# Performance work log

Hardware: AMD Instinct MI355X
Metric: run time of the kernel (lower is better)

## Reference

```python
import jax, jax.numpy as jnp
import numpy as np

B, N_PIC, C, H, W, P = 32, 4, 3, 224, 224, 16
HP = H // P  # 14
NP = HP * HP  # 196 patches
D = C * P * P  # 768 = hidden_size


def setup_inputs() -> dict:
    key = jax.random.key(0)
    ks = jax.random.split(key, 12)
    s = 0.02
    def lin(k, din, dout):
        kw, kb = jax.random.split(k)
        return (jax.random.normal(kw, (din, dout), jnp.float32) * s,
                jax.random.normal(kb, (dout,), jnp.float32) * s)
    W1, b1 = lin(ks[0], D, D)
    Wq, bq = lin(ks[1], D, D)
    Wk, bk = lin(ks[2], D, D)
    Wv, bv = lin(ks[3], D, D)
    Wo1, bo1 = lin(ks[4], D, D)
    Wo2, bo2 = lin(ks[5], D, D)
    x = jax.random.normal(ks[6], (B, N_PIC, C, H, W), jnp.float32)
    return {"x": x, "W1": W1, "b1": b1, "Wq": Wq, "bq": bq, "Wk": Wk,
            "bk": bk, "Wv": Wv, "bv": bv, "Wo1": Wo1, "bo1": bo1,
            "Wo2": Wo2, "bo2": bo2}


def reference(x, W1, b1, Wq, bq, Wk, bk, Wv, bv, Wo1, bo1, Wo2, bo2):
    b = x.shape[0]
    # patchify: matches torch unfold(3,P,P).unfold(4,P,P) + permute + view
    # -> [b, N, num_patches, C*P*P] with (C, ph, pw) ordering in last dim
    p = x.reshape(b, N_PIC, C, HP, P, HP, P)
    p = p.transpose(0, 1, 3, 5, 2, 4, 6).reshape(b, N_PIC, NP, D)
    h = p @ W1 + b1  # [b, N, S, D]
    # attention: query always from picture 0; key/value per picture (batched)
    Q = h[:, 0] @ Wq + bq          # [b, S, D]
    K = h @ Wk + bk                # [b, N, S, D]
    V = h @ Wv + bv                # [b, N, S, D]
    scale = 1.0 / jnp.sqrt(jnp.float32(D))
    scores = jnp.einsum('bsd,bnmd->bnsm', Q, K) * scale  # [b, N, S, S]
    attn = jax.nn.softmax(scores, axis=-1)
    wv = jnp.einsum('bnsm,bnmd->bnsd', attn, V)           # [b, N, S, D]
    out = jax.nn.relu(wv @ Wo1 + bo1) @ Wo2 + bo2
    return out
```

## Files before the change

kernel.cpp:

```cpp
#include <hip/hip_runtime.h>

typedef __bf16 bf16;
typedef __bf16 bf16x8 __attribute__((ext_vector_type(8)));
typedef float  f32x4  __attribute__((ext_vector_type(4)));


__global__ __launch_bounds__(256) void patchify_k(const float* __restrict__ x,
                                                  bf16* __restrict__ p) {
  int t = blockIdx.x * 256 + threadIdx.x;
  if (t >= 128 * 3 * 14 * 16 * 14) return;
  int j  = t % 14; t /= 14;
  int ph = t % 16; t /= 16;
  int i  = t % 14; t /= 14;
  int c  = t % 3;  t /= 3;
  int bn = t;
  const float* src = x + (((long long)(bn * 3 + c) * 224 + (i * 16 + ph)) * 224 + j * 16);
  bf16* dst = p + ((long long)(bn * 196 + (i * 14 + j)) * 768 + c * 256 + ph * 16);
  bf16 tmp[16];
  for (int k = 0; k < 16; k += 4) {
    float4 f = *(const float4*)(src + k);
    tmp[k + 0] = (bf16)f.x; tmp[k + 1] = (bf16)f.y;
    tmp[k + 2] = (bf16)f.z; tmp[k + 3] = (bf16)f.w;
  }
  *(bf16x8*)(dst)     = *(bf16x8*)&tmp[0];
  *(bf16x8*)(dst + 8) = *(bf16x8*)&tmp[8];
}

__global__ __launch_bounds__(256) void wtrans_k(const float* __restrict__ w0,
                                                const float* __restrict__ w1,
                                                const float* __restrict__ w2,
                                                const float* __restrict__ w3,
                                                const float* __restrict__ w4,
                                                const float* __restrict__ w5,
                                                bf16* __restrict__ out) {
  __shared__ float tile[32][33];
  const float* W;
  switch (blockIdx.z) {
    case 0: W = w0; break; case 1: W = w1; break; case 2: W = w2; break;
    case 3: W = w3; break; case 4: W = w4; break; default: W = w5; break;
  }
  bf16* o = out + (long long)blockIdx.z * 768 * 768;
  int nb = blockIdx.x * 32, kb = blockIdx.y * 32;
  int c = threadIdx.x & 31, r = threadIdx.x >> 5;
  for (int rr = 0; rr < 32; rr += 8)
    tile[r + rr][c] = W[(long long)(kb + r + rr) * 768 + nb + c];
  __syncthreads();
  for (int rr = 0; rr < 32; rr += 8)
    o[(long long)(nb + r + rr) * 768 + kb + c] = (bf16)tile[c][r + rr];
}

__global__ __launch_bounds__(256) void vtrans_k(const bf16* __restrict__ kv,
                                                bf16* __restrict__ Vt) {
  __shared__ short tile[32][33];
  int z = blockIdx.z;
  const short* v = (const short*)(kv + (long long)z * 301056 + 768);
  short* vt = (short*)(Vt + (long long)z * 768 * 224);
  int db = blockIdx.x * 32;
  int mb = blockIdx.y * 32;
  int c = threadIdx.x & 31, r = threadIdx.x >> 5;
  for (int rr = 0; rr < 32; rr += 8) {
    int m = mb + r + rr;
    short val = 0;
    if (m < 196) val = v[(long long)m * 1536 + db + c];
    tile[r + rr][c] = val;
  }
  __syncthreads();
  for (int rr = 0; rr < 32; rr += 8) {
    int d = db + r + rr;
    vt[(long long)d * 224 + mb + c] = tile[c][r + rr];
  }
}

__global__ __launch_bounds__(64) void softmax_k(const float* __restrict__ S,
                                                bf16* __restrict__ attn) {
  const int row = blockIdx.x;
  const float* sr = S + (long long)row * 196;
  const int l = threadIdx.x;
  float v0 = sr[l];
  float v1 = sr[l + 64];
  float v2 = sr[l + 128];
  float v3 = (l + 192 < 196) ? sr[l + 192] : -1e30f;
  float mx = fmaxf(fmaxf(v0, v1), fmaxf(v2, v3));
  for (int o = 32; o > 0; o >>= 1) mx = fmaxf(mx, __shfl_xor(mx, o));
  float e0 = __expf(v0 - mx);
  float e1 = __expf(v1 - mx);
  float e2 = __expf(v2 - mx);
  float e3 = (l + 192 < 196) ? __expf(v3 - mx) : 0.f;
  float s = e0 + e1 + e2 + e3;
  for (int o = 32; o > 0; o >>= 1) s += __shfl_xor(s, o);
  float inv = 1.0f / s;
  bf16* ar = attn + (long long)row * 224;
  ar[l]       = (bf16)(e0 * inv);
  ar[l + 64]  = (bf16)(e1 * inv);
  ar[l + 128] = (bf16)(e2 * inv);
  int m3 = l + 192;
  if (m3 < 196) ar[m3] = (bf16)(e3 * inv);
  else if (m3 < 224) ar[m3] = (bf16)0.0f;
}

__device__ __forceinline__ void gld16(const bf16* g, bf16* l) {
  __builtin_amdgcn_global_load_lds(
      (const __attribute__((address_space(1))) unsigned int*)g,
      (__attribute__((address_space(3))) unsigned int*)l, 16, 0, 0);
}

__global__ __launch_bounds__(256) void gemm128(
    const bf16* __restrict__ A, const bf16* __restrict__ Bt,
    const float* __restrict__ bias, const float* __restrict__ bias2,
    void* __restrict__ Cout,
    int M, int N, int K, int lda, int ldb, int gr, long long gs,
    long long strideAz, int a_zdiv, long long strideBz, long long strideCz,
    float scale, int relu, int out_bf16) {
  __shared__ __align__(16) char smem[34816];
  bf16* AsBuf = (bf16*)smem;
  bf16* BsBuf = (bf16*)(smem + 16384);

  const int tid = threadIdx.x;
  const int lane = tid & 63;
  const int w = tid >> 6;
  const int wm = w & 1, wn = w >> 1;
  const int z = blockIdx.z;
  const int n0 = blockIdx.x * 128, m0 = blockIdx.y * 128;

  const bf16* Az  = A  + (long long)(z / a_zdiv) * strideAz;
  const bf16* Btz = Bt + (long long)z * strideBz;

  const int rl  = 16 * w + (lane & 15);
  const int kc8 = (lane >> 4) * 8;
  int ar0 = m0 + rl;        if (ar0 >= M) ar0 = M - 1;
  int ar1 = m0 + 64 + rl;   if (ar1 >= M) ar1 = M - 1;
  const bf16* aP0 = Az + (long long)(ar0 / gr) * gs + (long long)(ar0 % gr) * lda + kc8;
  const bf16* aP1 = Az + (long long)(ar1 / gr) * gs + (long long)(ar1 % gr) * lda + kc8;
  int br0 = n0 + rl;        if (br0 >= N) br0 = N - 1;
  int br1 = n0 + 64 + rl;   if (br1 >= N) br1 = N - 1;
  const bf16* bP0 = Btz + (long long)br0 * ldb + kc8;
  const bf16* bP1 = Btz + (long long)br1 * ldb + kc8;

  const int dstOff = w * 512;

#define ISSUE(t, buf) do { const int _o = (t) << 5;                 \
    gld16(aP0 + _o, AsBuf + (buf) * 4096 + dstOff);                 \
    gld16(aP1 + _o, AsBuf + (buf) * 4096 + 2048 + dstOff);          \
    gld16(bP0 + _o, BsBuf + (buf) * 4096 + dstOff);                 \
    gld16(bP1 + _o, BsBuf + (buf) * 4096 + 2048 + dstOff); } while (0)

  const int niter = K >> 5;
  f32x4 acc[4][4] = {};
  const int fr = lane & 15, fq = lane >> 4;

  ISSUE(0, 0);

  for (int i = 0; i < niter; ++i) {
    __syncthreads();
    const int cur = i & 1;
    if (i + 1 < niter) ISSUE(i + 1, cur ^ 1);

    const bf16* Ac = AsBuf + cur * 4096;
    const bf16* Bc = BsBuf + cur * 4096;
    bf16x8 a[4], b[4];
#pragma unroll
    for (int mi = 0; mi < 4; mi++)
      a[mi] = *(const bf16x8*)&Ac[(wm * 4 + mi) * 512 + fq * 128 + fr * 8];
#pragma unroll
    for (int ni = 0; ni < 4; ni++)
      b[ni] = *(const bf16x8*)&Bc[(wn * 4 + ni) * 512 + fq * 128 + fr * 8];
#pragma unroll
    for (int mi = 0; mi < 4; mi++)
#pragma unroll
      for (int ni = 0; ni < 4; ni++)
        acc[mi][ni] = __builtin_amdgcn_mfma_f32_16x16x32_bf16(a[mi], b[ni], acc[mi][ni], 0, 0, 0);
  }
#undef ISSUE

  __syncthreads();

  const long long cz = (long long)z * strideCz;
  if (out_bf16) {
    bf16* Cs = (bf16*)smem;
#pragma unroll
    for (int ni = 0; ni < 4; ni++) {
      int col = wn * 64 + ni * 16 + fr;
      int gcol = n0 + col;
      float bb = 0.f;
      if (bias) bb = (bias2 && gcol >= 768) ? bias2[gcol - 768] : bias[gcol];
#pragma unroll
      for (int mi = 0; mi < 4; mi++) {
        int rbase = wm * 64 + mi * 16 + fq * 4;
#pragma unroll
        for (int r = 0; r < 4; r++) {
          float v = acc[mi][ni][r] * scale + bb;
          if (relu) v = fmaxf(v, 0.f);
          Cs[(rbase + r) * 136 + col] = (bf16)v;
        }
      }
    }
    __syncthreads();
    bf16* Cp = (bf16*)Cout;
    const int rr = tid >> 4, cc = (tid & 15) * 8;
#pragma unroll
    for (int pp = 0; pp < 8; pp++) {
      int row = pp * 16 + rr;
      int grow = m0 + row;
      if (grow < M)
        *(bf16x8*)(Cp + cz + (long long)grow * N + n0 + cc) =
            *(const bf16x8*)&Cs[row * 136 + cc];
    }
  } else {
    float* Cs = (float*)smem;
    float* Cp = (float*)Cout;
    for (int half = 0; half < 2; ++half) {
      if (wm == half) {
#pragma unroll
        for (int ni = 0; ni < 4; ni++) {
          int col = wn * 64 + ni * 16 + fr;
          int gcol = n0 + col;
          float bb = 0.f;
          if (bias && gcol < N)
            bb = (bias2 && gcol >= 768) ? bias2[gcol - 768] : bias[gcol];
#pragma unroll
          for (int mi = 0; mi < 4; mi++) {
            int rbase = mi * 16 + fq * 4;
#pragma unroll
            for (int r = 0; r < 4; r++) {
              float v = acc[mi][ni][r] * scale + bb;
              if (relu) v = fmaxf(v, 0.f);
              Cs[(rbase + r) * 132 + col] = v;
            }
          }
        }
      }
      __syncthreads();
      const int rr = tid >> 5, cc = (tid & 31) * 4;
#pragma unroll
      for (int pp = 0; pp < 8; pp++) {
        int row = pp * 8 + rr;
        int grow = m0 + half * 64 + row;
        if (grow < M) {
          int gcol = n0 + cc;
          float* dst = Cp + cz + (long long)grow * N + gcol;
          const float* srcl = &Cs[row * 132 + cc];
          if (gcol + 4 <= N) {
            *(float4*)dst = *(const float4*)srcl;
          } else {
            for (int e = 0; e < 4; e++)
              if (gcol + e < N) dst[e] = srcl[e];
          }
        }
      }
      __syncthreads();
    }
  }
}

__global__ __launch_bounds__(512, 2) void gemm256(
    const bf16* __restrict__ A, const bf16* __restrict__ Bt,
    const float* __restrict__ bias, const float* __restrict__ bias2,
    void* __restrict__ Cout,
    int N, int K, int lda, int ldb, int relu, int out_bf16) {
  __shared__ __align__(16) char smem[131072];
  bf16* As = (bf16*)smem;
  bf16* Bs = (bf16*)(smem + 65536);

  const int tid = threadIdx.x;
  const int lane = tid & 63;
  const int w = tid >> 6;
  const int wm = w >> 2;
  const int wn = w & 3;

  const int nx = N >> 8;
  const int nwg = gridDim.x * gridDim.y;
  int f = blockIdx.y * gridDim.x + blockIdx.x;
  {
    const int q = nwg >> 3, r = nwg & 7;
    const int xcd = f & 7, idx = f >> 3;
    f = (xcd < r ? xcd * (q + 1) : r * (q + 1) + (xcd - r) * q) + idx;
  }
  const int n0 = (f % nx) * 256;
  const int m0 = (f / nx) * 256;

  const int srow = ((tid >> 2) & 15) + ((tid >> 7) << 4);
  const int scol = ((tid >> 6) & 1) * 32 +
                   (((tid & 3) << 3) ^ ((tid & 32) ? 16 : 0));
  const bf16* aBase = A  + (long long)(m0 + srow) * lda + scol;
  const bf16* bBase = Bt + (long long)(n0 + srow) * ldb + scol;
  const int ldsw = w * 512;

#define STGQ(base, ld, dstArr, buf, kt, hh, q)                               \
  gld16((base) + (long long)((hh) * 128 + (q) * 64) * (ld) + (kt) * 64,      \
        (dstArr) + (buf) * 16384 + (hh) * 8192 + (q) * 4096 + ldsw)

  const int fr = lane & 15, fq = lane >> 4;
  const int frij = fr * 32 + ((fq * 8) ^ ((fr & 8) ? 16 : 0));
  const bf16* aRd = As + wm * 8192 + frij;
  const bf16* bRd = Bs + (wn >> 1) * 8192 + (wn & 1) * 4096 + frij;

  f32x4 acc[8][4] = {};
  bf16x8 A0f[4][2], A1f[4][2], B0f[2][2], B1f[2][2];

  const int nt = K >> 6;

  STGQ(aBase, lda, As, 0, 0, 0, 0); STGQ(aBase, lda, As, 0, 0, 1, 0);
  STGQ(aBase, lda, As, 0, 0, 0, 1); STGQ(aBase, lda, As, 0, 0, 1, 1);
  STGQ(bBase, ldb, Bs, 0, 0, 0, 0); STGQ(bBase, ldb, Bs, 0, 0, 0, 1);
  STGQ(bBase, ldb, Bs, 0, 0, 1, 0); STGQ(bBase, ldb, Bs, 0, 0, 1, 1);
  if (nt > 1) {
    STGQ(aBase, lda, As, 1, 1, 0, 0); STGQ(aBase, lda, As, 1, 1, 1, 0);
    STGQ(bBase, ldb, Bs, 1, 1, 0, 0); STGQ(bBase, ldb, Bs, 1, 1, 0, 1);
    STGQ(bBase, ldb, Bs, 1, 1, 1, 0); STGQ(bBase, ldb, Bs, 1, 1, 1, 1);
    STGQ(aBase, lda, As, 1, 1, 0, 1); STGQ(aBase, lda, As, 1, 1, 1, 1);
  }
  asm volatile("s_waitcnt vmcnt(0)" ::: "memory");
  asm volatile("s_barrier" ::: "memory");
#pragma unroll
  for (int mi = 0; mi < 4; ++mi)
#pragma unroll
    for (int kk = 0; kk < 2; ++kk)
      A0f[mi][kk] = *(const bf16x8*)(aRd + mi * 1024 + kk * 512);
#pragma unroll
  for (int ni = 0; ni < 2; ++ni)
#pragma unroll
    for (int kk = 0; kk < 2; ++kk)
      B0f[ni][kk] = *(const bf16x8*)(bRd + ni * 1024 + kk * 512);
  asm volatile("s_waitcnt lgkmcnt(0)" ::: "memory");
  asm volatile("s_barrier" ::: "memory");

  for (int t = 0; t < nt; ++t) {
    const int bo = (t & 1) << 14;
    const int bn = ((t & 1) ^ 1) << 14;
    const int b = t & 1;

#pragma unroll
    for (int ni = 0; ni < 2; ++ni)
#pragma unroll
      for (int kk = 0; kk < 2; ++kk)
        B1f[ni][kk] = *(const bf16x8*)(bRd + bo + (2 + ni) * 1024 + kk * 512);
    if (t + 2 < nt) {
      STGQ(aBase, lda, As, b, t + 2, 0, 0);
      STGQ(aBase, lda, As, b, t + 2, 1, 0);
      asm volatile("s_waitcnt vmcnt(2)" ::: "memory");
    } else {
      asm volatile("s_waitcnt vmcnt(0)" ::: "memory");
    }
    asm volatile("s_barrier" ::: "memory");
    __builtin_amdgcn_s_setprio(1);
#pragma unroll
    for (int mi = 0; mi < 4; ++mi)
#pragma unroll
      for (int ni = 0; ni < 2; ++ni)
#pragma unroll
        for (int kk = 0; kk < 2; ++kk)
          acc[mi][ni] = __builtin_amdgcn_mfma_f32_16x16x32_bf16(
              A0f[mi][kk], B0f[ni][kk], acc[mi][ni], 0, 0, 0);
    __builtin_amdgcn_s_setprio(0);
    asm volatile("s_barrier" ::: "memory");

#pragma unroll
    for (int mi = 0; mi < 4; ++mi)
#pragma unroll
      for (int kk = 0; kk < 2; ++kk)
        A1f[mi][kk] = *(const bf16x8*)(aRd + bo + (4 + mi) * 1024 + kk * 512);
    asm volatile("s_barrier" ::: "memory");
    __builtin_amdgcn_s_setprio(1);
#pragma unroll
    for (int mi = 0; mi < 4; ++mi)
#pragma unroll
      for (int ni = 0; ni < 2; ++ni)
#pragma unroll
        for (int kk = 0; kk < 2; ++kk)
          acc[mi][2 + ni] = __builtin_amdgcn_mfma_f32_16x16x32_bf16(
              A0f[mi][kk], B1f[ni][kk], acc[mi][2 + ni], 0, 0, 0);
    __builtin_amdgcn_s_setprio(0);
    asm volatile("s_barrier" ::: "memory");

    if (t + 1 < nt) {
#pragma unroll
      for (int mi = 0; mi < 4; ++mi)
#pragma unroll
        for (int kk = 0; kk < 2; ++kk)
          A0f[mi][kk] = *(const bf16x8*)(aRd + bn + mi * 1024 + kk * 512);
    }
    if (t + 2 < nt) {
      STGQ(bBase, ldb, Bs, b, t + 2, 0, 0);
      STGQ(bBase, ldb, Bs, b, t + 2, 0, 1);
      STGQ(bBase, ldb, Bs, b, t + 2, 1, 0);
      STGQ(bBase, ldb, Bs, b, t + 2, 1, 1);
    }
    asm volatile("s_barrier" ::: "memory");
    __builtin_amdgcn_s_setprio(1);
#pragma unroll
    for (int mi = 0; mi < 4; ++mi)
#pragma unroll
      for (int ni = 0; ni < 2; ++ni)
#pragma unroll
        for (int kk = 0; kk < 2; ++kk)
          acc[4 + mi][ni] = __builtin_amdgcn_mfma_f32_16x16x32_bf16(
              A1f[mi][kk], B0f[ni][kk], acc[4 + mi][ni], 0, 0, 0);
    __builtin_amdgcn_s_setprio(0);
    asm volatile("s_barrier" ::: "memory");

    if (t + 1 < nt) {
#pragma unroll
      for (int ni = 0; ni < 2; ++ni)
#pragma unroll
        for (int kk = 0; kk < 2; ++kk)
          B0f[ni][kk] = *(const bf16x8*)(bRd + bn + ni * 1024 + kk * 512);
    }
    if (t + 2 < nt) {
      STGQ(aBase, lda, As, b, t + 2, 0, 1);
      STGQ(aBase, lda, As, b, t + 2, 1, 1);
    }
    asm volatile("s_barrier" ::: "memory");
    __builtin_amdgcn_s_setprio(1);
#pragma unroll
    for (int mi = 0; mi < 4; ++mi)
#pragma unroll
      for (int ni = 0; ni < 2; ++ni)
#pragma unroll
        for (int kk = 0; kk < 2; ++kk)
          acc[4 + mi][2 + ni] = __builtin_amdgcn_mfma_f32_16x16x32_bf16(
              A1f[mi][kk], B1f[ni][kk], acc[4 + mi][2 + ni], 0, 0, 0);
    __builtin_amdgcn_s_setprio(0);
    asm volatile("s_barrier" ::: "memory");
  }
#undef STGQ

  const long long Nll = N;
  if (out_bf16) {
    bf16* Cs = (bf16*)smem;
    bf16* Cp = (bf16*)Cout;
#pragma unroll
    for (int half = 0; half < 2; ++half) {
      if (wm == half) {
#pragma unroll
        for (int ni = 0; ni < 4; ++ni) {
          const int col = wn * 64 + ni * 16 + fr;
          const int gcol = n0 + col;
          float bb = 0.f;
          if (bias) bb = (bias2 && gcol >= 768) ? bias2[gcol - 768] : bias[gcol];
#pragma unroll
          for (int mi = 0; mi < 8; ++mi) {
#pragma unroll
            for (int r = 0; r < 4; ++r) {
              float v = acc[mi][ni][r] + bb;
              if (relu) v = fmaxf(v, 0.f);
              Cs[(mi * 16 + fq * 4 + r) * 268 + col] = (bf16)v;
            }
          }
        }
      }
      __syncthreads();
      const int row = tid >> 2, cb = (tid & 3) * 8;
      const bf16* srcl = &Cs[row * 268 + cb];
      bf16* dst = Cp + (long long)(m0 + half * 128 + row) * Nll + n0 + cb;
#pragma unroll
      for (int j = 0; j < 8; ++j)
        *(bf16x8*)(dst + j * 32) = *(const bf16x8*)(srcl + j * 32);
      __syncthreads();
    }
  } else {
    float* Cs = (float*)smem;
    float* Cp = (float*)Cout;
#pragma unroll
    for (int pass = 0; pass < 4; ++pass) {
      if (wm == (pass >> 1)) {
#pragma unroll
        for (int ni = 0; ni < 4; ++ni) {
          const int col = wn * 64 + ni * 16 + fr;
          const int gcol = n0 + col;
          float bb = 0.f;
          if (bias) bb = (bias2 && gcol >= 768) ? bias2[gcol - 768] : bias[gcol];
#pragma unroll
          for (int mi2 = 0; mi2 < 4; ++mi2) {
            const int mi = (pass & 1) * 4 + mi2;
#pragma unroll
            for (int r = 0; r < 4; ++r) {
              float v = acc[mi][ni][r] + bb;
              if (relu) v = fmaxf(v, 0.f);
              Cs[(mi2 * 16 + fq * 4 + r) * 268 + col] = v;
            }
          }
        }
      }
      __syncthreads();
      const int row = tid >> 3, c4 = (tid & 7) * 4;
      const float* srcl = &Cs[row * 268 + c4];
      float* dst = Cp + (long long)(m0 + pass * 64 + row) * Nll + n0 + c4;
#pragma unroll
      for (int j = 0; j < 8; ++j)
        *(float4*)(dst + j * 32) = *(const float4*)(srcl + j * 32);
      __syncthreads();
    }
  }
}

extern "C" void kernel_launch(void* const* d_in, const int* in_sizes, int n_in,
                              void* d_out, int out_size, void* d_ws, size_t ws_size,
                              hipStream_t stream) {
  (void)in_sizes; (void)n_in; (void)out_size; (void)ws_size;
  const float* x   = (const float*)d_in[0];
  const float* W1  = (const float*)d_in[1];
  const float* b1  = (const float*)d_in[2];
  const float* Wq  = (const float*)d_in[3];
  const float* bq  = (const float*)d_in[4];
  const float* Wk  = (const float*)d_in[5];
  const float* bk  = (const float*)d_in[6];
  const float* Wv  = (const float*)d_in[7];
  const float* bv  = (const float*)d_in[8];
  const float* Wo1 = (const float*)d_in[9];
  const float* bo1 = (const float*)d_in[10];
  const float* Wo2 = (const float*)d_in[11];
  const float* bo2 = (const float*)d_in[12];

  char* ws = (char*)d_ws;
  bf16*  p    = (bf16*)(ws + 0);
  bf16*  vt   = (bf16*)(ws + 0);
  bf16*  h    = (bf16*)(ws + 44040192LL);
  bf16*  wv   = (bf16*)(ws + 44040192LL);
  bf16*  kv   = (bf16*)(ws + 82575360LL);
  bf16*  o1   = (bf16*)(ws + 82575360LL);
  float* sc   = (float*)(ws + 159645696LL);
  bf16*  q    = (bf16*)(ws + 179314688LL);
  bf16*  attn = (bf16*)(ws + 179314688LL);
  bf16*  wt   = (bf16*)(ws + 190554112LL);
  constexpr long long WSZ = 768LL * 768;

  const float qk_scale = 0.03608439182435161f;

  patchify_k<<<4704, 256, 0, stream>>>(x, p);
  wtrans_k<<<dim3(24, 24, 6), 256, 0, stream>>>(W1, Wk, Wv, Wq, Wo1, Wo2, wt);

  gemm256<<<dim3(3, 98), 512, 0, stream>>>(p, wt + 0 * WSZ, b1, nullptr, h,
      768, 768, 768, 768, 0, 1);
  gemm256<<<dim3(6, 98), 512, 0, stream>>>(h, wt + 1 * WSZ, bk, bv, kv,
      1536, 768, 768, 768, 0, 1);
  gemm128<<<dim3(6, 49, 1), 256, 0, stream>>>(h, wt + 3 * WSZ, bq, nullptr, q,
      6272, 768, 768, 768, 768, 196, 602112LL, 0LL, 1, 0LL, 0LL, 1.f, 0, 1);
  vtrans_k<<<dim3(24, 7, 128), 256, 0, stream>>>(kv, vt);
  gemm128<<<dim3(2, 2, 128), 256, 0, stream>>>(q, kv, nullptr, nullptr, sc,
      196, 196, 768, 768, 1536, 196, 0LL, 150528LL, 4, 301056LL, 38416LL,
      qk_scale, 0, 0);
  softmax_k<<<25088, 64, 0, stream>>>(sc, attn);
  gemm128<<<dim3(6, 2, 128), 256, 0, stream>>>(attn, vt, nullptr, nullptr, wv,
      196, 768, 224, 224, 224, 196, 0LL, 43904LL, 1, 172032LL, 150528LL,
      1.f, 0, 1);
  gemm256<<<dim3(3, 98), 512, 0, stream>>>(wv, wt + 4 * WSZ, bo1, nullptr, o1,
      768, 768, 768, 768, 1, 1);
  gemm256<<<dim3(3, 98), 512, 0, stream>>>(o1, wt + 5 * WSZ, bo2, nullptr,
      (float*)d_out, 768, 768, 768, 768, 0, 0);
}
```

Before: 561.3 us.

## Reorder GEMM global-to-LDS stage issue to match consumption and relax vmcnt waits

Reorders the prologue and in-loop global-to-LDS copies so each quarter tile is issued in the order the fragments are read. The single full vmcnt(0) wait is replaced by finer partial waits placed just before each dependent LDS read. The aim is to keep more loads in flight and hide memory latency behind the MFMA blocks. Getting the vmcnt counts wrong could cause stale reads, and the prologue now assumes nt>1 without a guard.

```diff
diff --git a/kernel.cpp b/kernel.cpp
--- a/kernel.cpp
+++ b/kernel.cpp
@@ -300,16 +300,14 @@
   const int nt = K >> 6;
 
   STGQ(aBase, lda, As, 0, 0, 0, 0); STGQ(aBase, lda, As, 0, 0, 1, 0);
+  STGQ(bBase, ldb, Bs, 0, 0, 1, 0); STGQ(bBase, ldb, Bs, 0, 0, 1, 1);
   STGQ(aBase, lda, As, 0, 0, 0, 1); STGQ(aBase, lda, As, 0, 0, 1, 1);
   STGQ(bBase, ldb, Bs, 0, 0, 0, 0); STGQ(bBase, ldb, Bs, 0, 0, 0, 1);
-  STGQ(bBase, ldb, Bs, 0, 0, 1, 0); STGQ(bBase, ldb, Bs, 0, 0, 1, 1);
-  if (nt > 1) {
-    STGQ(aBase, lda, As, 1, 1, 0, 0); STGQ(aBase, lda, As, 1, 1, 1, 0);
-    STGQ(bBase, ldb, Bs, 1, 1, 0, 0); STGQ(bBase, ldb, Bs, 1, 1, 0, 1);
-    STGQ(bBase, ldb, Bs, 1, 1, 1, 0); STGQ(bBase, ldb, Bs, 1, 1, 1, 1);
-    STGQ(aBase, lda, As, 1, 1, 0, 1); STGQ(aBase, lda, As, 1, 1, 1, 1);
-  }
-  asm volatile("s_waitcnt vmcnt(0)" ::: "memory");
+  STGQ(aBase, lda, As, 1, 1, 0, 0); STGQ(aBase, lda, As, 1, 1, 1, 0);
+  STGQ(bBase, ldb, Bs, 1, 1, 1, 0); STGQ(bBase, ldb, Bs, 1, 1, 1, 1);
+  STGQ(aBase, lda, As, 1, 1, 0, 1); STGQ(aBase, lda, As, 1, 1, 1, 1);
+  STGQ(bBase, ldb, Bs, 1, 1, 0, 0); STGQ(bBase, ldb, Bs, 1, 1, 0, 1);
+  asm volatile("s_waitcnt vmcnt(8)" ::: "memory");
   asm volatile("s_barrier" ::: "memory");
 #pragma unroll
   for (int mi = 0; mi < 4; ++mi)
@@ -322,25 +320,23 @@
     for (int kk = 0; kk < 2; ++kk)
       B0f[ni][kk] = *(const bf16x8*)(bRd + ni * 1024 + kk * 512);
   asm volatile("s_waitcnt lgkmcnt(0)" ::: "memory");
+  __builtin_amdgcn_sched_barrier(0);
   asm volatile("s_barrier" ::: "memory");
 
   for (int t = 0; t < nt; ++t) {
     const int bo = (t & 1) << 14;
     const int bn = ((t & 1) ^ 1) << 14;
     const int b = t & 1;
+    const bool stg = (t + 2 < nt);
+    const bool nxt = (t + 1 < nt);
 
 #pragma unroll
     for (int ni = 0; ni < 2; ++ni)
 #pragma unroll
       for (int kk = 0; kk < 2; ++kk)
         B1f[ni][kk] = *(const bf16x8*)(bRd + bo + (2 + ni) * 1024 + kk * 512);
-    if (t + 2 < nt) {
-      STGQ(aBase, lda, As, b, t + 2, 0, 0);
-      STGQ(aBase, lda, As, b, t + 2, 1, 0);
-      asm volatile("s_waitcnt vmcnt(2)" ::: "memory");
-    } else {
-      asm volatile("s_waitcnt vmcnt(0)" ::: "memory");
-    }
+    if (stg) { STGQ(aBase, lda, As, b, t + 2, 0, 0);
+               STGQ(aBase, lda, As, b, t + 2, 1, 0); }
     asm volatile("s_barrier" ::: "memory");
     __builtin_amdgcn_s_setprio(1);
 #pragma unroll
@@ -359,6 +355,8 @@
 #pragma unroll
       for (int kk = 0; kk < 2; ++kk)
         A1f[mi][kk] = *(const bf16x8*)(aRd + bo + (4 + mi) * 1024 + kk * 512);
+    if (stg) { STGQ(bBase, ldb, Bs, b, t + 2, 1, 0);
+               STGQ(bBase, ldb, Bs, b, t + 2, 1, 1); }
     asm volatile("s_barrier" ::: "memory");
     __builtin_amdgcn_s_setprio(1);
 #pragma unroll
@@ -370,21 +368,19 @@
           acc[mi][2 + ni] = __builtin_amdgcn_mfma_f32_16x16x32_bf16(
               A0f[mi][kk], B1f[ni][kk], acc[mi][2 + ni], 0, 0, 0);
     __builtin_amdgcn_s_setprio(0);
-    asm volatile("s_barrier" ::: "memory");
-
-    if (t + 1 < nt) {
+    if (stg) asm volatile("s_waitcnt vmcnt(6)" ::: "memory");
+    else     asm volatile("s_waitcnt vmcnt(2)" ::: "memory");
+    asm volatile("s_barrier" ::: "memory");
+
+    if (nxt) {
 #pragma unroll
       for (int mi = 0; mi < 4; ++mi)
 #pragma unroll
         for (int kk = 0; kk < 2; ++kk)
           A0f[mi][kk] = *(const bf16x8*)(aRd + bn + mi * 1024 + kk * 512);
     }
-    if (t + 2 < nt) {
-      STGQ(bBase, ldb, Bs, b, t + 2, 0, 0);
-      STGQ(bBase, ldb, Bs, b, t + 2, 0, 1);
-      STGQ(bBase, ldb, Bs, b, t + 2, 1, 0);
-      STGQ(bBase, ldb, Bs, b, t + 2, 1, 1);
-    }
+    if (stg) { STGQ(aBase, lda, As, b, t + 2, 0, 1);
+               STGQ(aBase, lda, As, b, t + 2, 1, 1); }
     asm volatile("s_barrier" ::: "memory");
     __builtin_amdgcn_s_setprio(1);
 #pragma unroll
@@ -396,19 +392,19 @@
           acc[4 + mi][ni] = __builtin_amdgcn_mfma_f32_16x16x32_bf16(
               A1f[mi][kk], B0f[ni][kk], acc[4 + mi][ni], 0, 0, 0);
     __builtin_amdgcn_s_setprio(0);
-    asm volatile("s_barrier" ::: "memory");
-
-    if (t + 1 < nt) {
+    if (stg) asm volatile("s_waitcnt vmcnt(6)" ::: "memory");
+    else     asm volatile("s_waitcnt vmcnt(0)" ::: "memory");
+    asm volatile("s_barrier" ::: "memory");
+
+    if (nxt) {
 #pragma unroll
       for (int ni = 0; ni < 2; ++ni)
 #pragma unroll
         for (int kk = 0; kk < 2; ++kk)
           B0f[ni][kk] = *(const bf16x8*)(bRd + bn + ni * 1024 + kk * 512);
     }
-    if (t + 2 < nt) {
-      STGQ(aBase, lda, As, b, t + 2, 0, 1);
-      STGQ(aBase, lda, As, b, t + 2, 1, 1);
-    }
+    if (stg) { STGQ(bBase, ldb, Bs, b, t + 2, 0, 0);
+               STGQ(bBase, ldb, Bs, b, t + 2, 0, 1); }
     asm volatile("s_barrier" ::: "memory");
     __builtin_amdgcn_s_setprio(1);
 #pragma unroll
```

New measurement: 560.0 us. No clear change (-0.2%).
